# Kernel optimization log

Hardware: AMD Instinct MI355X
Metric: run time of the kernel (lower is better)

Reference implementation:

```python
import jax, jax.numpy as jnp
import numpy as np

N_NODES = 100000
N_EDGES = 1600000
IN_DIM = 256
OUT_DIM = 128


def setup_inputs() -> dict:
    key = jax.random.key(0)
    k1, k2, k3, k4 = jax.random.split(key, 4)
    x = jax.random.normal(k1, (N_NODES, IN_DIM), dtype=jnp.float32)
    edge_list = jax.random.randint(k2, (2, N_EDGES), 0, N_NODES, dtype=jnp.int64)
    # xavier_uniform with gain=1.414
    gW = 1.414 * np.sqrt(6.0 / (IN_DIM + OUT_DIM))
    W = jax.random.uniform(k3, (IN_DIM, OUT_DIM), dtype=jnp.float32, minval=-gW, maxval=gW)
    ga = 1.414 * np.sqrt(6.0 / (2 * OUT_DIM + 1))
    a = jax.random.uniform(k4, (2 * OUT_DIM, 1), dtype=jnp.float32, minval=-ga, maxval=ga)
    return {"x": x, "edge_list": edge_list, "W": W, "a": a}


def reference(x, edge_list, W, a):
    N = x.shape[0]
    src, dst = edge_list[0], edge_list[1]
    h = x @ W  # [N, out_dim]
    # cat([h[src], h[dst]]) @ a  ==  h[src] @ a[:d] + h[dst] @ a[d:]
    d = h.shape[1]
    s_src = (h @ a[:d]).ravel()  # [N]
    s_dst = (h @ a[d:]).ravel()  # [N]
    e = jax.nn.leaky_relu(s_src[src] + s_dst[dst], negative_slope=0.2)  # [E]
    # sparse softmax over rows (segments = src node)
    seg_max = jax.ops.segment_max(e, src, num_segments=N)  # [N]
    ex = jnp.exp(e - seg_max[src])  # [E]
    denom = jax.ops.segment_sum(ex, src, num_segments=N)  # [N]
    attn = ex / jnp.where(denom > 0, denom, 1.0)[src]  # [E]
    # sparse aggregate: h_prime[i] = sum_{edges (i,j)} attn_ij * h[j]
    h_prime = jax.ops.segment_sum(attn[:, None] * h[dst], src, num_segments=N)  # [N, d]
    return jax.nn.elu(h_prime)
```

## Files before the change

### kernel.cpp

```cpp
#include <hip/hip_runtime.h>
#include <hip/hip_bf16.h>
#include <cstdint>
#include <cstddef>

#define NN 100000
#define NE 1600000
#define KD 256
#define OD 128
#define NB 391
#define CAP 8192
#define NGB 782

typedef __attribute__((ext_vector_type(8))) __bf16 bf16x8;
typedef __attribute__((ext_vector_type(4))) float f32x4;
typedef __attribute__((ext_vector_type(8))) unsigned short ushort8;

static __device__ __forceinline__ unsigned short f2bf(float f) {
  return __builtin_bit_cast(unsigned short, (__bf16)f);
}
static __device__ __forceinline__ float bflo(unsigned p) {
  return __builtin_bit_cast(float, p << 16);
}
static __device__ __forceinline__ float bfhi(unsigned p) {
  return __builtin_bit_cast(float, p & 0xffff0000u);
}

__global__ void prep_wt_k(const float* __restrict__ W, unsigned short* __restrict__ Wt,
                          int* __restrict__ bcur) {
  const int i = blockIdx.x * 256 + threadIdx.x;
  const int k = i >> 7;
  const int n = i & 127;
  Wt[n * KD + k] = f2bf(W[i]);
  if (i < NB) bcur[i] = i * CAP;
}

__global__ __launch_bounds__(512, 4) void fused_k(
    const float* __restrict__ x, const unsigned short* __restrict__ Wt,
    const float* __restrict__ a, unsigned short* __restrict__ h,
    float* __restrict__ ssrc, float* __restrict__ sdst,
    const int* __restrict__ el, int* __restrict__ bcur,
    unsigned* __restrict__ stage) {
  __shared__ alignas(16) char smem[65536];
  const int t = threadIdx.x;

  if (blockIdx.x < NGB) {
    unsigned short* Bl = (unsigned short*)smem;
#pragma unroll
    for (int it = 0; it < 8; ++it) {
      const int c = it * 512 + t;
      const int r = c >> 5;
      const int c16 = c & 31;
      const ushort8 v = *(const ushort8*)(Wt + r * 256 + c16 * 8);
      const int byt = (r * 512 + c16 * 16) ^ ((r & 7) << 4);
      *(ushort8*)((char*)Bl + byt) = v;
    }
    const int lane = t & 63;
    const int wave = t >> 6;
    const int col = lane & 15;
    const int kg = lane >> 4;
    const int m0 = blockIdx.x * 128 + wave * 16;
    const int arow = m0 + col;
    const bool rowok = arow < NN;
    const float* __restrict__ xrow = x + (size_t)arow * KD;
    __syncthreads();

    f32x4 acc[8];
#pragma unroll
    for (int i = 0; i < 8; ++i) acc[i] = (f32x4)0.0f;

#pragma unroll
    for (int s = 0; s < 8; ++s) {
      const int kk = s * 32 + kg * 8;
      bf16x8 af = (bf16x8)(__bf16)0.0f;
      if (rowok) {
        const float4 f0 = *(const float4*)(xrow + kk);
        const float4 f1 = *(const float4*)(xrow + kk + 4);
        af[0] = (__bf16)f0.x; af[1] = (__bf16)f0.y; af[2] = (__bf16)f0.z; af[3] = (__bf16)f0.w;
        af[4] = (__bf16)f1.x; af[5] = (__bf16)f1.y; af[6] = (__bf16)f1.z; af[7] = (__bf16)f1.w;
      }
#pragma unroll
      for (int nt = 0; nt < 8; ++nt) {
        const int n = nt * 16 + col;
        const int byt = (n * 512 + s * 64 + kg * 16) ^ ((col & 7) << 4);
        const ushort8 bu = *(const ushort8*)((const char*)Bl + byt);
        const bf16x8 bf = __builtin_bit_cast(bf16x8, bu);
        acc[nt] = __builtin_amdgcn_mfma_f32_16x16x32_bf16(af, bf, acc[nt], 0, 0, 0);
      }
    }

    float ps[4] = {0.f, 0.f, 0.f, 0.f};
    float pd[4] = {0.f, 0.f, 0.f, 0.f};
#pragma unroll
    for (int nt = 0; nt < 8; ++nt) {
      const int n = nt * 16 + col;
      const float av = a[n];
      const float av2 = a[OD + n];
#pragma unroll
      for (int r = 0; r < 4; ++r) {
        const float v = acc[nt][r];
        const int row = m0 + kg * 4 + r;
        if (row < NN) h[(size_t)row * OD + n] = f2bf(v);
        ps[r] += v * av;
        pd[r] += v * av2;
      }
    }
#pragma unroll
    for (int off = 1; off < 16; off <<= 1) {
#pragma unroll
      for (int r = 0; r < 4; ++r) {
        ps[r] += __shfl_xor(ps[r], off, 64);
        pd[r] += __shfl_xor(pd[r], off, 64);
      }
    }
    if (col == 0) {
#pragma unroll
      for (int r = 0; r < 4; ++r) {
        const int row = m0 + kg * 4 + r;
        if (row < NN) {
          ssrc[row] = ps[r] * 1.442695041f;
          sdst[row] = pd[r] * 1.442695041f;
        }
      }
    }
  } else {
    unsigned* sorted = (unsigned*)smem;
    unsigned short* bkid = (unsigned short*)(smem + 16384);
    int* hist  = (int*)(smem + 24576);
    int* off   = (int*)(smem + 26144);
    int* cur   = (int*)(smem + 27712);
    int* delta = (int*)(smem + 29276);
    const int te = (blockIdx.x - NGB) * 4096 + t * 8;
    int s[8], d[8];
    bool valid[8];
#pragma unroll
    for (int u = 0; u < 8; ++u) valid[u] = (te + u) < NE;
    if (te + 7 < NE) {
      const int4 a0 = *(const int4*)(el + te);
      const int4 a1 = *(const int4*)(el + te + 4);
      const int4 b0 = *(const int4*)(el + NE + te);
      const int4 b1 = *(const int4*)(el + NE + te + 4);
      s[0] = a0.x; s[1] = a0.y; s[2] = a0.z; s[3] = a0.w;
      s[4] = a1.x; s[5] = a1.y; s[6] = a1.z; s[7] = a1.w;
      d[0] = b0.x; d[1] = b0.y; d[2] = b0.z; d[3] = b0.w;
      d[4] = b1.x; d[5] = b1.y; d[6] = b1.z; d[7] = b1.w;
    } else {
#pragma unroll
      for (int u = 0; u < 8; ++u) {
        s[u] = valid[u] ? el[te + u] : 0;
        d[u] = valid[u] ? el[NE + te + u] : 0;
      }
    }
    for (int i = t; i <= NB; i += 512) hist[i] = 0;
    __syncthreads();
#pragma unroll
    for (int u = 0; u < 8; ++u)
      if (valid[u]) atomicAdd(&hist[s[u] >> 8], 1);
    __syncthreads();
    if (t < 64) {
      int v[7];
      int sum = 0;
#pragma unroll
      for (int i = 0; i < 7; ++i) {
        const int idx = t * 7 + i;
        v[i] = (idx <= NB) ? hist[idx] : 0;
        sum += v[i];
      }
      int pre = sum;
#pragma unroll
      for (int o = 1; o < 64; o <<= 1) {
        const int nb = __shfl_up(pre, o, 64);
        if (t >= o) pre += nb;
      }
      pre -= sum;
      int run = pre;
#pragma unroll
      for (int i = 0; i < 7; ++i) {
        const int idx = t * 7 + i;
        if (idx <= NB) off[idx] = run;
        run += v[i];
      }
    }
    __syncthreads();
    for (int i = t; i < NB; i += 512) cur[i] = off[i];
    __syncthreads();
#pragma unroll
    for (int u = 0; u < 8; ++u)
      if (valid[u]) {
        const int b = s[u] >> 8;
        const int p = atomicAdd(&cur[b], 1);
        sorted[p] = ((unsigned)(s[u] & 255) << 17) | (unsigned)d[u];
        bkid[p] = (unsigned short)b;
      }
    __syncthreads();
    for (int b = t; b < NB; b += 512) {
      const int len = off[b + 1] - off[b];
      if (len > 0) {
        const int gb = atomicAdd(&bcur[b], len);
        delta[b] = gb - off[b];
      }
    }
    __syncthreads();
    const int n = off[NB];
    for (int i = t; i < n; i += 512) {
      const int b = bkid[i];
      const int pos = delta[b] + i;
      if (pos < (b + 1) * CAP) stage[pos] = sorted[i];
    }
  }
}

__global__ __launch_bounds__(512) void bscan_k(const int* __restrict__ bcur,
                                               int* __restrict__ bbase) {
  __shared__ int tmp[512];
  const int t = threadIdx.x;
  int v = 0;
  if (t < NB) {
    v = bcur[t] - t * CAP;
    v = v > CAP ? CAP : v;
  }
  tmp[t] = v;
  __syncthreads();
  for (int o = 1; o < 512; o <<= 1) {
    const int add = (t >= o) ? tmp[t - o] : 0;
    __syncthreads();
    tmp[t] += add;
    __syncthreads();
  }
  if (t < NB) bbase[t] = tmp[t] - v;
}

__global__ __launch_bounds__(256) void place2_k(const unsigned* __restrict__ stage,
                                                const int* __restrict__ bcur,
                                                const int* __restrict__ bbase,
                                                const float* __restrict__ ssrc,
                                                const float* __restrict__ sdst,
                                                unsigned* __restrict__ csrw,
                                                int* __restrict__ cnt,
                                                int* __restrict__ rowstart) {
  __shared__ unsigned ebuf[CAP];
  __shared__ float sl[256];
  __shared__ int hist2[256];
  __shared__ int exc[256];
  __shared__ int cur2[256];
  const int b = blockIdx.x;
  const int t = threadIdx.x;
  int tot = bcur[b] - b * CAP;
  tot = tot > CAP ? CAP : tot;
  const int base = bbase[b];
  const int node = b * 256 + t;
  hist2[t] = 0;
  sl[t] = (node < NN) ? ssrc[node] : 0.f;
  for (int i = t; i < tot; i += 256) ebuf[i] = stage[(size_t)b * CAP + i];
  __syncthreads();
  for (int i = t; i < tot; i += 256) atomicAdd(&hist2[ebuf[i] >> 17], 1);
  __syncthreads();
  if (t < 64) {
    int v[4];
    int sum = 0;
#pragma unroll
    for (int i = 0; i < 4; ++i) { v[i] = hist2[t * 4 + i]; sum += v[i]; }
    int pre = sum;
#pragma unroll
    for (int o = 1; o < 64; o <<= 1) {
      const int nb = __shfl_up(pre, o, 64);
      if (t >= o) pre += nb;
    }
    pre -= sum;
    int run = pre;
#pragma unroll
    for (int i = 0; i < 4; ++i) { exc[t * 4 + i] = run; run += v[i]; }
  }
  __syncthreads();
  if (node < NN) {
    cnt[node] = hist2[t];
    rowstart[node] = base + exc[t];
  }
  cur2[t] = exc[t];
  __syncthreads();
  for (int i = t; i < tot; i += 256) {
    const unsigned u = ebuf[i];
    const int s = u >> 17;
    const unsigned d = u & 0x1ffffu;
    const float sv = sl[s] + sdst[d];
    const float w = exp2f(fmaxf(sv, 0.2f * sv));
    unsigned wb = __builtin_bit_cast(unsigned, w);
    wb += 0x7fffu + ((wb >> 16) & 1u);
    const unsigned ent = ((wb >> 16) << 17) | d;
    const int p = atomicAdd(&cur2[s], 1);
    csrw[base + p] = ent;
  }
}

__global__ __launch_bounds__(256) void aggr_k(
    const unsigned short* __restrict__ h, const unsigned* __restrict__ csrw,
    const int* __restrict__ rowstart, const int* __restrict__ cnt,
    float* __restrict__ out) {
  const int lane = threadIdx.x & 63;
  const int g = lane >> 4;
  const int sub = lane & 15;
  const int node = blockIdx.x * 4 + (threadIdx.x >> 6);
  const int r0 = rowstart[node];
  const int deg = cnt[node];
  const int jend = r0 + deg;
  const uint4* __restrict__ hp = (const uint4*)h;
  float acc[8] = {0.f, 0.f, 0.f, 0.f, 0.f, 0.f, 0.f, 0.f};
  float sw = 0.f;
  const int nit = (deg + 7) >> 3;
  for (int it = 0; it < nit; ++it) {
    const int j0 = r0 + it * 8 + g;
    const int j1 = j0 + 4;
    const unsigned u0 = csrw[j0 < jend ? j0 : r0];
    const unsigned u1 = csrw[j1 < jend ? j1 : r0];
    const unsigned d0 = u0 & 0x1ffffu;
    const unsigned d1 = u1 & 0x1ffffu;
    const uint4 p0 = hp[d0 * 16u + sub];
    const uint4 p1 = hp[d1 * 16u + sub];
    const float w0 = (j0 < jend) ? __builtin_bit_cast(float, (u0 >> 17) << 16) : 0.f;
    const float w1 = (j1 < jend) ? __builtin_bit_cast(float, (u1 >> 17) << 16) : 0.f;
    sw += w0 + w1;
    const unsigned k0[4] = {p0.x, p0.y, p0.z, p0.w};
    const unsigned k1[4] = {p1.x, p1.y, p1.z, p1.w};
#pragma unroll
    for (int q = 0; q < 4; ++q) {
      acc[q * 2]     = fmaf(w0, bflo(k0[q]), fmaf(w1, bflo(k1[q]), acc[q * 2]));
      acc[q * 2 + 1] = fmaf(w0, bfhi(k0[q]), fmaf(w1, bfhi(k1[q]), acc[q * 2 + 1]));
    }
  }
#pragma unroll
  for (int off = 16; off < 64; off <<= 1) {
    sw += __shfl_xor(sw, off, 64);
#pragma unroll
    for (int q = 0; q < 8; ++q) acc[q] += __shfl_xor(acc[q], off, 64);
  }
  const float inv = deg > 0 ? 1.0f / sw : 0.f;
  float o[8];
#pragma unroll
  for (int q = 0; q < 8; ++q) {
    const float v = acc[q] * inv;
    o[q] = v > 0.f ? v : __expf(v) - 1.f;
  }
  if (lane < 16) {
    float4* op = (float4*)(out + (size_t)node * OD + sub * 8);
    op[0] = make_float4(o[0], o[1], o[2], o[3]);
    op[1] = make_float4(o[4], o[5], o[6], o[7]);
  }
}

extern "C" void kernel_launch(void* const* d_in, const int* in_sizes, int n_in,
                              void* d_out, int out_size, void* d_ws, size_t ws_size,
                              hipStream_t stream) {
  const float* x = (const float*)d_in[0];
  const int* el = (const int*)d_in[1];
  const float* W = (const float*)d_in[2];
  const float* a = (const float*)d_in[3];
  float* out = (float*)d_out;
  char* ws = (char*)d_ws;

  const size_t S = 400384;
  float* ssrc    = (float*)(ws + 0 * S);
  float* sdst    = (float*)(ws + 1 * S);
  int* cnt       = (int*)(ws + 2 * S);
  int* rowstart  = (int*)(ws + 3 * S);
  int* bcur      = (int*)(ws + 4 * S);
  int* bbase     = (int*)(ws + 4 * S + 2048);
  unsigned short* Wt = (unsigned short*)(ws + 4 * S + 8192);
  unsigned short* h  = (unsigned short*)(ws + 4 * S + 8192 + 65536);
  unsigned* csrw = (unsigned*)(ws + 4 * S + 8192 + 65536 + (size_t)NN * OD * 2);
  unsigned* stage = (unsigned*)d_out;

  prep_wt_k<<<128, 256, 0, stream>>>(W, Wt, bcur);
  fused_k<<<NGB + NB, 512, 0, stream>>>(x, Wt, a, h, ssrc, sdst, el, bcur, stage);
  bscan_k<<<1, 512, 0, stream>>>(bcur, bbase);
  place2_k<<<NB, 256, 0, stream>>>(stage, bcur, bbase, ssrc, sdst, csrw, cnt, rowstart);
  aggr_k<<<NN / 4, 256, 0, stream>>>(h, csrw, rowstart, cnt, out);
}
```

Baseline: 122.1 us.

## Fold block scan into place kernel, pack row info, prefetch next edges in aggregation

Removes the single-block bscan kernel launch: each place2 block now computes its own base by reducing the clamped bucket counts of earlier buckets. Per-node count and row start are packed into one uint2 so the aggregation kernel does a single load instead of two. The aggregation loop is software-pipelined, issuing the next iteration's index and gathered h loads before the current FMAs run, to hide gather latency. In exchange, every place2 block redundantly re-reads the bucket counts, and the prefetch raises register pressure in aggr_k.

```diff
diff --git a/kernel.cpp b/kernel.cpp
--- a/kernel.cpp
+++ b/kernel.cpp
@@ -209,47 +209,39 @@
   }
 }
 
-__global__ __launch_bounds__(512) void bscan_k(const int* __restrict__ bcur,
-                                               int* __restrict__ bbase) {
-  __shared__ int tmp[512];
-  const int t = threadIdx.x;
-  int v = 0;
-  if (t < NB) {
-    v = bcur[t] - t * CAP;
-    v = v > CAP ? CAP : v;
-  }
-  tmp[t] = v;
-  __syncthreads();
-  for (int o = 1; o < 512; o <<= 1) {
-    const int add = (t >= o) ? tmp[t - o] : 0;
-    __syncthreads();
-    tmp[t] += add;
-    __syncthreads();
-  }
-  if (t < NB) bbase[t] = tmp[t] - v;
-}
-
 __global__ __launch_bounds__(256) void place2_k(const unsigned* __restrict__ stage,
                                                 const int* __restrict__ bcur,
-                                                const int* __restrict__ bbase,
                                                 const float* __restrict__ ssrc,
                                                 const float* __restrict__ sdst,
                                                 unsigned* __restrict__ csrw,
-                                                int* __restrict__ cnt,
-                                                int* __restrict__ rowstart) {
+                                                uint2* __restrict__ rc) {
   __shared__ unsigned ebuf[CAP];
   __shared__ float sl[256];
   __shared__ int hist2[256];
   __shared__ int exc[256];
   __shared__ int cur2[256];
+  __shared__ int red[256];
+  __shared__ int tot_s;
   const int b = blockIdx.x;
   const int t = threadIdx.x;
-  int tot = bcur[b] - b * CAP;
-  tot = tot > CAP ? CAP : tot;
-  const int base = bbase[b];
   const int node = b * 256 + t;
+  int partial = 0;
+  for (int i = t; i < NB; i += 256) {
+    int c = bcur[i] - i * CAP;
+    c = c > CAP ? CAP : c;
+    if (i == b) tot_s = c;
+    if (i < b) partial += c;
+  }
+  red[t] = partial;
   hist2[t] = 0;
   sl[t] = (node < NN) ? ssrc[node] : 0.f;
+  __syncthreads();
+  for (int o = 128; o > 0; o >>= 1) {
+    if (t < o) red[t] += red[t + o];
+    __syncthreads();
+  }
+  const int base = red[0];
+  const int tot = tot_s;
   for (int i = t; i < tot; i += 256) ebuf[i] = stage[(size_t)b * CAP + i];
   __syncthreads();
   for (int i = t; i < tot; i += 256) atomicAdd(&hist2[ebuf[i] >> 17], 1);
@@ -271,10 +263,7 @@
     for (int i = 0; i < 4; ++i) { exc[t * 4 + i] = run; run += v[i]; }
   }
   __syncthreads();
-  if (node < NN) {
-    cnt[node] = hist2[t];
-    rowstart[node] = base + exc[t];
-  }
+  if (node < NN) rc[node] = make_uint2((unsigned)hist2[t], (unsigned)(base + exc[t]));
   cur2[t] = exc[t];
   __syncthreads();
   for (int i = t; i < tot; i += 256) {
@@ -293,37 +282,50 @@
 
 __global__ __launch_bounds__(256) void aggr_k(
     const unsigned short* __restrict__ h, const unsigned* __restrict__ csrw,
-    const int* __restrict__ rowstart, const int* __restrict__ cnt,
-    float* __restrict__ out) {
+    const uint2* __restrict__ rc, float* __restrict__ out) {
   const int lane = threadIdx.x & 63;
   const int g = lane >> 4;
   const int sub = lane & 15;
   const int node = blockIdx.x * 4 + (threadIdx.x >> 6);
-  const int r0 = rowstart[node];
-  const int deg = cnt[node];
+  const uint2 rcv = rc[node];
+  const int deg = (int)rcv.x;
+  const int r0 = (int)rcv.y;
   const int jend = r0 + deg;
   const uint4* __restrict__ hp = (const uint4*)h;
   float acc[8] = {0.f, 0.f, 0.f, 0.f, 0.f, 0.f, 0.f, 0.f};
   float sw = 0.f;
   const int nit = (deg + 7) >> 3;
-  for (int it = 0; it < nit; ++it) {
-    const int j0 = r0 + it * 8 + g;
-    const int j1 = j0 + 4;
-    const unsigned u0 = csrw[j0 < jend ? j0 : r0];
-    const unsigned u1 = csrw[j1 < jend ? j1 : r0];
-    const unsigned d0 = u0 & 0x1ffffu;
-    const unsigned d1 = u1 & 0x1ffffu;
-    const uint4 p0 = hp[d0 * 16u + sub];
-    const uint4 p1 = hp[d1 * 16u + sub];
-    const float w0 = (j0 < jend) ? __builtin_bit_cast(float, (u0 >> 17) << 16) : 0.f;
-    const float w1 = (j1 < jend) ? __builtin_bit_cast(float, (u1 >> 17) << 16) : 0.f;
-    sw += w0 + w1;
-    const unsigned k0[4] = {p0.x, p0.y, p0.z, p0.w};
-    const unsigned k1[4] = {p1.x, p1.y, p1.z, p1.w};
-#pragma unroll
-    for (int q = 0; q < 4; ++q) {
-      acc[q * 2]     = fmaf(w0, bflo(k0[q]), fmaf(w1, bflo(k1[q]), acc[q * 2]));
-      acc[q * 2 + 1] = fmaf(w0, bfhi(k0[q]), fmaf(w1, bfhi(k1[q]), acc[q * 2 + 1]));
+  if (nit > 0) {
+    int j0 = r0 + g, j1 = j0 + 4;
+    bool vA0 = j0 < jend, vA1 = j1 < jend;
+    unsigned uA0 = csrw[vA0 ? j0 : r0];
+    unsigned uA1 = csrw[vA1 ? j1 : r0];
+    uint4 pA0 = hp[(uA0 & 0x1ffffu) * 16u + sub];
+    uint4 pA1 = hp[(uA1 & 0x1ffffu) * 16u + sub];
+    for (int it = 0; it < nit; ++it) {
+      unsigned uB0 = 0, uB1 = 0;
+      uint4 pB0, pB1;
+      bool vB0 = false, vB1 = false;
+      if (it + 1 < nit) {
+        const int k0 = r0 + (it + 1) * 8 + g;
+        const int k1 = k0 + 4;
+        vB0 = k0 < jend; vB1 = k1 < jend;
+        uB0 = csrw[vB0 ? k0 : r0];
+        uB1 = csrw[vB1 ? k1 : r0];
+        pB0 = hp[(uB0 & 0x1ffffu) * 16u + sub];
+        pB1 = hp[(uB1 & 0x1ffffu) * 16u + sub];
+      }
+      const float w0 = vA0 ? __builtin_bit_cast(float, (uA0 >> 17) << 16) : 0.f;
+      const float w1 = vA1 ? __builtin_bit_cast(float, (uA1 >> 17) << 16) : 0.f;
+      sw += w0 + w1;
+      const unsigned k0a[4] = {pA0.x, pA0.y, pA0.z, pA0.w};
+      const unsigned k1a[4] = {pA1.x, pA1.y, pA1.z, pA1.w};
+#pragma unroll
+      for (int q = 0; q < 4; ++q) {
+        acc[q * 2]     = fmaf(w0, bflo(k0a[q]), fmaf(w1, bflo(k1a[q]), acc[q * 2]));
+        acc[q * 2 + 1] = fmaf(w0, bfhi(k0a[q]), fmaf(w1, bfhi(k1a[q]), acc[q * 2 + 1]));
+      }
+      uA0 = uB0; uA1 = uB1; pA0 = pB0; pA1 = pB1; vA0 = vB0; vA1 = vB1;
     }
   }
 #pragma unroll
@@ -359,10 +361,8 @@
   const size_t S = 400384;
   float* ssrc    = (float*)(ws + 0 * S);
   float* sdst    = (float*)(ws + 1 * S);
-  int* cnt       = (int*)(ws + 2 * S);
-  int* rowstart  = (int*)(ws + 3 * S);
+  uint2* rc      = (uint2*)(ws + 2 * S);
   int* bcur      = (int*)(ws + 4 * S);
-  int* bbase     = (int*)(ws + 4 * S + 2048);
   unsigned short* Wt = (unsigned short*)(ws + 4 * S + 8192);
   unsigned short* h  = (unsigned short*)(ws + 4 * S + 8192 + 65536);
   unsigned* csrw = (unsigned*)(ws + 4 * S + 8192 + 65536 + (size_t)NN * OD * 2);
@@ -370,7 +370,6 @@
 
   prep_wt_k<<<128, 256, 0, stream>>>(W, Wt, bcur);
   fused_k<<<NGB + NB, 512, 0, stream>>>(x, Wt, a, h, ssrc, sdst, el, bcur, stage);
-  bscan_k<<<1, 512, 0, stream>>>(bcur, bbase);
-  place2_k<<<NB, 256, 0, stream>>>(stage, bcur, bbase, ssrc, sdst, csrw, cnt, rowstart);
-  aggr_k<<<NN / 4, 256, 0, stream>>>(h, csrw, rowstart, cnt, out);
-}
+  place2_k<<<NB, 256, 0, stream>>>(stage, bcur, ssrc, sdst, csrw, rc);
+  aggr_k<<<NN / 4, 256, 0, stream>>>(h, csrw, rc, out);
+}
```

After: 119.0 us. 1.03x faster.
